# Kernel tuning notes

Measured on AMD Instinct MI355X. Metric: run time of the kernel, lower is better.

The kernel has to match this reference:

```python
import jax, jax.numpy as jnp
import numpy as np

B, N, IN_DIM, OUT_DIM = 8, 2048, 256, 256
EDGE_P = 0.02   # adjacency density
MASK_P = 0.9    # fraction of valid nodes


def setup_inputs() -> dict:
    key = jax.random.key(0)
    ks = jax.random.split(key, 8)
    x = jax.random.normal(ks[0], (B, N, IN_DIM), dtype=jnp.float32)
    adj = (jax.random.uniform(ks[1], (B, N, N)) < EDGE_P).astype(jnp.float32)
    mask = (jax.random.uniform(ks[2], (B, N)) < MASK_P).astype(jnp.float32)
    # nn.Linear(in_dim, out_dim): W [out, in], b [out]
    lim1 = 1.0 / np.sqrt(IN_DIM)
    W = jax.random.uniform(ks[3], (OUT_DIM, IN_DIM), minval=-lim1, maxval=lim1, dtype=jnp.float32)
    b = jax.random.uniform(ks[4], (OUT_DIM,), minval=-lim1, maxval=lim1, dtype=jnp.float32)
    # nn.Linear(2*out_dim, 1): weight [1, 2D] split into a1 (acts on h_i), a2 (acts on h_j)
    lim2 = 1.0 / np.sqrt(2 * OUT_DIM)
    a1 = jax.random.uniform(ks[5], (OUT_DIM,), minval=-lim2, maxval=lim2, dtype=jnp.float32)
    a2 = jax.random.uniform(ks[6], (OUT_DIM,), minval=-lim2, maxval=lim2, dtype=jnp.float32)
    att_b = jax.random.uniform(ks[7], (), minval=-lim2, maxval=lim2, dtype=jnp.float32)
    return {"x": x, "adj": adj, "mask": mask, "W": W, "b": b, "a1": a1, "a2": a2, "att_b": att_b}


def reference(x, adj, mask, W, b, a1, a2, att_b):
    # h = Linear(x): [B, N, D]
    h = jnp.einsum('bni,di->bnd', x, W) + b
    # attention(cat([h_i, h_j])) == h_i @ a1 + h_j @ a2 + att_b (linear in each half)
    s1 = h @ a1  # [B, N] -> contributes along i
    s2 = h @ a2  # [B, N] -> contributes along j
    logits = s1[:, :, None] + s2[:, None, :] + att_b  # [B, N, N]
    att = jax.nn.sigmoid(logits) * adj
    att = att * mask[:, :, None] * mask[:, None, :]
    att = att / (jnp.sum(att, axis=-1, keepdims=True) + 1e-8)
    h_new = jnp.einsum('bij,bjd->bid', att, h)
    return h_new * mask[:, :, None]
```

## Files before the change

### kernel.cpp

```cpp
#include <hip/hip_runtime.h>
#include <hip/hip_bf16.h>

#define BB 8
#define NN 2048
#define DD 256
#define MM (BB * NN)

typedef __attribute__((ext_vector_type(8))) short bf16x8_t;
typedef __attribute__((ext_vector_type(4))) float f32x4_t;

__global__ __launch_bounds__(256) void gemm_h(
    const float* __restrict__ x,
    const float* __restrict__ Wt,
    const float* __restrict__ bias,
    __hip_bfloat16* __restrict__ h)
{
    __shared__ __hip_bfloat16 As[64][72];
    __shared__ __hip_bfloat16 Bs[64][72];

    const int tid  = threadIdx.x;
    const int r    = tid >> 2;
    const int cs   = (tid & 3) * 16;
    const int w    = tid >> 6;
    const int lane = tid & 63;
    const int m16  = lane & 15;
    const int quad = lane >> 4;
    const long rowBase = (long)blockIdx.x * 64;
    const int  colBase = blockIdx.y * 64;

    f32x4_t acc[4];
#pragma unroll
    for (int c = 0; c < 4; c++) acc[c] = (f32x4_t){0.f, 0.f, 0.f, 0.f};

    for (int k0 = 0; k0 < 256; k0 += 64) {
        const float4* ag = (const float4*)(x  + (rowBase + r) * 256 + k0 + cs);
        const float4* bg = (const float4*)(Wt + (long)(colBase + r) * 256 + k0 + cs);
        float4 av[4], bv[4];
#pragma unroll
        for (int q = 0; q < 4; q++) { av[q] = ag[q]; bv[q] = bg[q]; }

        __align__(16) __hip_bfloat16 ta[16], tb[16];
#pragma unroll
        for (int q = 0; q < 4; q++) {
            ta[q * 4 + 0] = __float2bfloat16(av[q].x);
            ta[q * 4 + 1] = __float2bfloat16(av[q].y);
            ta[q * 4 + 2] = __float2bfloat16(av[q].z);
            ta[q * 4 + 3] = __float2bfloat16(av[q].w);
            tb[q * 4 + 0] = __float2bfloat16(bv[q].x);
            tb[q * 4 + 1] = __float2bfloat16(bv[q].y);
            tb[q * 4 + 2] = __float2bfloat16(bv[q].z);
            tb[q * 4 + 3] = __float2bfloat16(bv[q].w);
        }

        __syncthreads();
        *(uint4*)&As[r][cs]     = *(uint4*)&ta[0];
        *(uint4*)&As[r][cs + 8] = *(uint4*)&ta[8];
        *(uint4*)&Bs[r][cs]     = *(uint4*)&tb[0];
        *(uint4*)&Bs[r][cs + 8] = *(uint4*)&tb[8];
        __syncthreads();

#pragma unroll
        for (int kk = 0; kk < 64; kk += 32) {
            bf16x8_t af = *(const bf16x8_t*)&As[w * 16 + m16][kk + quad * 8];
#pragma unroll
            for (int c = 0; c < 4; c++) {
                bf16x8_t bf = *(const bf16x8_t*)&Bs[c * 16 + m16][kk + quad * 8];
                acc[c] = __builtin_amdgcn_mfma_f32_16x16x32_bf16(af, bf, acc[c], 0, 0, 0);
            }
        }
    }

#pragma unroll
    for (int c = 0; c < 4; c++) {
        const int col = colBase + c * 16 + m16;
        const float bv = bias[col];
#pragma unroll
        for (int reg = 0; reg < 4; reg++) {
            const long row = rowBase + w * 16 + quad * 4 + reg;
            h[row * 256 + col] = __float2bfloat16(acc[c][reg] + bv);
        }
    }
}

struct __attribute__((aligned(8))) bf4 { __hip_bfloat16 v[4]; };

__global__ __launch_bounds__(256) void s_kernel(
    const __hip_bfloat16* __restrict__ h,
    const float* __restrict__ a1,
    const float* __restrict__ a2,
    const float* __restrict__ mask,
    const float* __restrict__ attb_p,
    float* __restrict__ s1b, float* __restrict__ t2)
{
    const int w = threadIdx.x >> 6;
    const int lane = threadIdx.x & 63;
    const long row = (long)blockIdx.x * 4 + w;

    bf4 hv = *(const bf4*)(h + row * 256 + lane * 4);
    float4 A1 = *(const float4*)(a1 + lane * 4);
    float4 A2 = *(const float4*)(a2 + lane * 4);
    const float h0 = __bfloat162float(hv.v[0]), h1 = __bfloat162float(hv.v[1]);
    const float h2 = __bfloat162float(hv.v[2]), h3 = __bfloat162float(hv.v[3]);
    float p1 = h0 * A1.x + h1 * A1.y + h2 * A1.z + h3 * A1.w;
    float p2 = h0 * A2.x + h1 * A2.y + h2 * A2.z + h3 * A2.w;
#pragma unroll
    for (int off = 32; off; off >>= 1) {
        p1 += __shfl_down(p1, off);
        p2 += __shfl_down(p2, off);
    }
    if (lane == 0) {
        s1b[row] = p1 + attb_p[0];
        t2[row]  = (mask[row] != 0.f) ? p2 : -1e30f;
    }
}

__global__ __launch_bounds__(256, 8) void attn_agg(
    const float* __restrict__ adj,
    const float* __restrict__ mask,
    const __hip_bfloat16* __restrict__ h,
    const float* __restrict__ s1b,
    const float* __restrict__ t2,
    float* __restrict__ out)
{
    __shared__ float2 s_list[2048];
    __shared__ int    s_cnt;
    __shared__ float  s_sum[4];

    const int tid  = threadIdx.x;
    const int wv   = tid >> 6;
    const int lane = tid & 63;
    const int b    = blockIdx.x & 7;
    const int i    = blockIdx.x >> 3;
    const long row   = (long)b * NN + i;
    const long mbase = (long)b * NN;

    const float mask_i = mask[row];
    if (mask_i == 0.f) {
        out[row * 256 + tid] = 0.f;
        return;
    }
    if (tid == 0) s_cnt = 0;
    __syncthreads();

    const float si = s1b[row];
    const float4* arow = (const float4*)(adj + row * NN);
    const float4* trow = (const float4*)(t2 + mbase);

    float4 A0 = arow[tid], A1 = arow[256 + tid];
    float4 T0 = trow[tid], T1 = trow[256 + tid];

    float lsum = 0.f;
#pragma unroll
    for (int g = 0; g < 2; g++) {
        const int jb = (g * 1024 + tid * 4) << 9;
        const float av[4] = {g ? A1.x : A0.x, g ? A1.y : A0.y, g ? A1.z : A0.z, g ? A1.w : A0.w};
        const float tv[4] = {g ? T1.x : T0.x, g ? T1.y : T0.y, g ? T1.z : T0.z, g ? T1.w : T0.w};
#pragma unroll
        for (int e = 0; e < 4; e++) {
            const float z   = si + tv[e];
            const float sig = __builtin_amdgcn_rcpf(1.f + __expf(-z));
            const float wgt = av[e] * sig;
            lsum += wgt;
            if (wgt != 0.f) {
                const int pos = atomicAdd(&s_cnt, 1);
                s_list[pos] = make_float2(__int_as_float(jb + (e << 9)), wgt);
            }
        }
    }

#pragma unroll
    for (int off = 32; off; off >>= 1) lsum += __shfl_down(lsum, off);
    if (lane == 0) s_sum[wv] = lsum;
    __syncthreads();

    const float inv = 1.f / (s_sum[0] + s_sum[1] + s_sum[2] + s_sum[3] + 1e-8f);
    const int   cnt = s_cnt;

    const char* hb   = (const char*)(h + mbase * 256);
    const int   coff = tid * 2;
    float acc = 0.f;
    int k = 0;
    for (; k + 8 <= cnt; k += 8) {
        float4 e[4];
#pragma unroll
        for (int q = 0; q < 4; q++) e[q] = *(const float4*)&s_list[k + q * 2];
        unsigned short u[8];
#pragma unroll
        for (int q = 0; q < 4; q++) {
            u[q * 2]     = *(const unsigned short*)(hb + __float_as_int(e[q].x) + coff);
            u[q * 2 + 1] = *(const unsigned short*)(hb + __float_as_int(e[q].z) + coff);
        }
#pragma unroll
        for (int q = 0; q < 4; q++) {
            acc += e[q].y * __uint_as_float(((unsigned)u[q * 2]) << 16);
            acc += e[q].w * __uint_as_float(((unsigned)u[q * 2 + 1]) << 16);
        }
    }
    for (; k + 2 <= cnt; k += 2) {
        float4 e = *(const float4*)&s_list[k];
        unsigned short u0 = *(const unsigned short*)(hb + __float_as_int(e.x) + coff);
        unsigned short u1 = *(const unsigned short*)(hb + __float_as_int(e.z) + coff);
        acc += e.y * __uint_as_float(((unsigned)u0) << 16);
        acc += e.w * __uint_as_float(((unsigned)u1) << 16);
    }
    if (k < cnt) {
        float2 e = s_list[k];
        unsigned short u = *(const unsigned short*)(hb + __float_as_int(e.x) + coff);
        acc += e.y * __uint_as_float(((unsigned)u) << 16);
    }

    out[row * 256 + tid] = acc * inv;
}

extern "C" void kernel_launch(void* const* d_in, const int* in_sizes, int n_in,
                              void* d_out, int out_size, void* d_ws, size_t ws_size,
                              hipStream_t stream) {
    const float* x    = (const float*)d_in[0];
    const float* adj  = (const float*)d_in[1];
    const float* mask = (const float*)d_in[2];
    const float* W    = (const float*)d_in[3];
    const float* bias = (const float*)d_in[4];
    const float* a1   = (const float*)d_in[5];
    const float* a2   = (const float*)d_in[6];
    const float* attb = (const float*)d_in[7];
    float* out = (float*)d_out;

    __hip_bfloat16* h = (__hip_bfloat16*)d_ws;
    float* s1b = (float*)((char*)d_ws + (size_t)MM * DD * 2);
    float* t2  = s1b + MM;

    gemm_h<<<dim3(MM / 64, DD / 64), 256, 0, stream>>>(x, W, bias, h);
    s_kernel<<<MM / 4, 256, 0, stream>>>(h, a1, a2, mask, attb, s1b, t2);
    attn_agg<<<MM, 256, 0, stream>>>(adj, mask, h, s1b, t2, out);
}
```

Before: 256.9 us.

## Split neighbor gather across wavefronts with 4-wide bf16 loads and LDS reduction

The aggregation loop now divides the neighbor list among the four wavefronts. Each lane loads 8 bytes (4 bf16 columns) per neighbor row instead of one 2-byte value, and the per-wave partial sums are combined through shared memory. The neighbor list is stored as separate ushort index and float weight arrays. This cuts the number of tiny global loads and the per-thread loop length, at the cost of an extra barrier, a 4 KB LDS partial buffer and higher LDS use that may lower occupancy.

After: 239.8 us. -6.6%, faster.

```diff
diff --git a/kernel.cpp b/kernel.cpp
--- a/kernel.cpp
+++ b/kernel.cpp
@@ -122,9 +122,11 @@
     const float* __restrict__ t2,
     float* __restrict__ out)
 {
-    __shared__ float2 s_list[2048];
-    __shared__ int    s_cnt;
-    __shared__ float  s_sum[4];
+    __shared__ unsigned short s_j[2048];
+    __shared__ float          s_w[2048];
+    __shared__ float          s_part[4][DD];
+    __shared__ int            s_cnt;
+    __shared__ float          s_sum[4];
 
     const int tid  = threadIdx.x;
     const int wv   = tid >> 6;
@@ -152,7 +154,7 @@
     float lsum = 0.f;
 #pragma unroll
     for (int g = 0; g < 2; g++) {
-        const int jb = (g * 1024 + tid * 4) << 9;
+        const int jb = g * 1024 + tid * 4;
         const float av[4] = {g ? A1.x : A0.x, g ? A1.y : A0.y, g ? A1.z : A0.z, g ? A1.w : A0.w};
         const float tv[4] = {g ? T1.x : T0.x, g ? T1.y : T0.y, g ? T1.z : T0.z, g ? T1.w : T0.w};
 #pragma unroll
@@ -163,7 +165,8 @@
             lsum += wgt;
             if (wgt != 0.f) {
                 const int pos = atomicAdd(&s_cnt, 1);
-                s_list[pos] = make_float2(__int_as_float(jb + (e << 9)), wgt);
+                s_j[pos] = (unsigned short)(jb + e);
+                s_w[pos] = wgt;
             }
         }
     }
@@ -176,40 +179,69 @@
     const float inv = 1.f / (s_sum[0] + s_sum[1] + s_sum[2] + s_sum[3] + 1e-8f);
     const int   cnt = s_cnt;
 
+    const int qs = ((cnt + 15) >> 4) << 2;
+    const int ks = min(wv * qs, cnt);
+    const int ke = min(ks + qs, cnt);
     const char* hb   = (const char*)(h + mbase * 256);
-    const int   coff = tid * 2;
-    float acc = 0.f;
-    int k = 0;
-    for (; k + 8 <= cnt; k += 8) {
-        float4 e[4];
-#pragma unroll
-        for (int q = 0; q < 4; q++) e[q] = *(const float4*)&s_list[k + q * 2];
-        unsigned short u[8];
+    const int   loff = lane * 8;
+
+    float c0 = 0.f, c1 = 0.f, c2 = 0.f, c3 = 0.f;
+    int k = ks;
+    for (; k + 8 <= ke; k += 8) {
+        ushort4 ja = *(const ushort4*)&s_j[k];
+        ushort4 jb2 = *(const ushort4*)&s_j[k + 4];
+        float4  wa = *(const float4*)&s_w[k];
+        float4  wb = *(const float4*)&s_w[k + 4];
+        uint2 u[8];
+        u[0] = *(const uint2*)(hb + ((int)ja.x  << 9) + loff);
+        u[1] = *(const uint2*)(hb + ((int)ja.y  << 9) + loff);
+        u[2] = *(const uint2*)(hb + ((int)ja.z  << 9) + loff);
+        u[3] = *(const uint2*)(hb + ((int)ja.w  << 9) + loff);
+        u[4] = *(const uint2*)(hb + ((int)jb2.x << 9) + loff);
+        u[5] = *(const uint2*)(hb + ((int)jb2.y << 9) + loff);
+        u[6] = *(const uint2*)(hb + ((int)jb2.z << 9) + loff);
+        u[7] = *(const uint2*)(hb + ((int)jb2.w << 9) + loff);
+        const float ww[8] = {wa.x, wa.y, wa.z, wa.w, wb.x, wb.y, wb.z, wb.w};
+#pragma unroll
+        for (int q = 0; q < 8; q++) {
+            c0 += ww[q] * __uint_as_float(u[q].x << 16);
+            c1 += ww[q] * __uint_as_float(u[q].x & 0xffff0000u);
+            c2 += ww[q] * __uint_as_float(u[q].y << 16);
+            c3 += ww[q] * __uint_as_float(u[q].y & 0xffff0000u);
+        }
+    }
+    for (; k + 4 <= ke; k += 4) {
+        ushort4 ja = *(const ushort4*)&s_j[k];
+        float4  wa = *(const float4*)&s_w[k];
+        uint2 u[4];
+        u[0] = *(const uint2*)(hb + ((int)ja.x << 9) + loff);
+        u[1] = *(const uint2*)(hb + ((int)ja.y << 9) + loff);
+        u[2] = *(const uint2*)(hb + ((int)ja.z << 9) + loff);
+        u[3] = *(const uint2*)(hb + ((int)ja.w << 9) + loff);
+        const float ww[4] = {wa.x, wa.y, wa.z, wa.w};
 #pragma unroll
         for (int q = 0; q < 4; q++) {
-            u[q * 2]     = *(const unsigned short*)(hb + __float_as_int(e[q].x) + coff);
-            u[q * 2 + 1] = *(const unsigned short*)(hb + __float_as_int(e[q].z) + coff);
-        }
-#pragma unroll
-        for (int q = 0; q < 4; q++) {
-            acc += e[q].y * __uint_as_float(((unsigned)u[q * 2]) << 16);
-            acc += e[q].w * __uint_as_float(((unsigned)u[q * 2 + 1]) << 16);
-        }
-    }
-    for (; k + 2 <= cnt; k += 2) {
-        float4 e = *(const float4*)&s_list[k];
-        unsigned short u0 = *(const unsigned short*)(hb + __float_as_int(e.x) + coff);
-        unsigned short u1 = *(const unsigned short*)(hb + __float_as_int(e.z) + coff);
-        acc += e.y * __uint_as_float(((unsigned)u0) << 16);
-        acc += e.w * __uint_as_float(((unsigned)u1) << 16);
-    }
-    if (k < cnt) {
-        float2 e = s_list[k];
-        unsigned short u = *(const unsigned short*)(hb + __float_as_int(e.x) + coff);
-        acc += e.y * __uint_as_float(((unsigned)u) << 16);
-    }
-
-    out[row * 256 + tid] = acc * inv;
+            c0 += ww[q] * __uint_as_float(u[q].x << 16);
+            c1 += ww[q] * __uint_as_float(u[q].x & 0xffff0000u);
+            c2 += ww[q] * __uint_as_float(u[q].y << 16);
+            c3 += ww[q] * __uint_as_float(u[q].y & 0xffff0000u);
+        }
+    }
+    for (; k < ke; k++) {
+        const int jj = s_j[k];
+        const float wk = s_w[k];
+        uint2 u = *(const uint2*)(hb + (jj << 9) + loff);
+        c0 += wk * __uint_as_float(u.x << 16);
+        c1 += wk * __uint_as_float(u.x & 0xffff0000u);
+        c2 += wk * __uint_as_float(u.y << 16);
+        c3 += wk * __uint_as_float(u.y & 0xffff0000u);
+    }
+
+    *(float4*)&s_part[wv][lane * 4] = make_float4(c0, c1, c2, c3);
+    __syncthreads();
+
+    const float total = s_part[0][tid] + s_part[1][tid] + s_part[2][tid] + s_part[3][tid];
+    out[row * 256 + tid] = total * inv;
 }
 
 extern "C" void kernel_launch(void* const* d_in, const int* in_sizes, int n_in,
```

## Replace sparse gather aggregation with dense MFMA attention matmul over transposed h

Applied to the files above, without the earlier changes.

The per-row sparse gather kernel, which compacted nonzero attention weights into shared memory and gathered h rows, is replaced by a dense tiled matmul. Each block builds a 32x64 bf16 tile of attention weights from adj and the sigmoid logits, then multiplies it with a transposed copy of h using MFMA. The GEMM now also writes that transposed copy. This removes the LDS atomics, the irregular scattered 2-byte loads and the one-block-per-row launch. In exchange it does about 50x more FLOPs, since the adjacency is only ~2% dense, rounds the attention weights to bf16, and computes masked rows instead of skipping them.

Measured after the change: 286.8 us. 11.7% more time.

```diff
diff --git a/kernel.cpp b/kernel.cpp
--- a/kernel.cpp
+++ b/kernel.cpp
@@ -13,7 +13,8 @@
     const float* __restrict__ x,
     const float* __restrict__ Wt,
     const float* __restrict__ bias,
-    __hip_bfloat16* __restrict__ h)
+    __hip_bfloat16* __restrict__ h,
+    __hip_bfloat16* __restrict__ hT)
 {
     __shared__ __hip_bfloat16 As[64][72];
     __shared__ __hip_bfloat16 Bs[64][72];
@@ -70,15 +71,21 @@
         }
     }
 
+    const long r0 = rowBase + w * 16 + quad * 4;
+    const int  bb = (int)(r0 >> 11);
+    const int  ib = (int)(r0 & 2047);
 #pragma unroll
     for (int c = 0; c < 4; c++) {
         const int col = colBase + c * 16 + m16;
         const float bv = bias[col];
-#pragma unroll
-        for (int reg = 0; reg < 4; reg++) {
-            const long row = rowBase + w * 16 + quad * 4 + reg;
-            h[row * 256 + col] = __float2bfloat16(acc[c][reg] + bv);
-        }
+        union { ushort4 u; __hip_bfloat16 b[4]; } pk;
+#pragma unroll
+        for (int reg = 0; reg < 4; reg++)
+            pk.b[reg] = __float2bfloat16(acc[c][reg] + bv);
+#pragma unroll
+        for (int reg = 0; reg < 4; reg++)
+            h[(r0 + reg) * 256 + col] = pk.b[reg];
+        *(ushort4*)((unsigned short*)hT + ((long)bb * 256 + col) * 2048 + ib) = pk.u;
     }
 }
 
@@ -114,102 +121,95 @@
     }
 }
 
-__global__ __launch_bounds__(256, 8) void attn_agg(
+__global__ __launch_bounds__(256, 2) void attn_mm(
     const float* __restrict__ adj,
     const float* __restrict__ mask,
-    const __hip_bfloat16* __restrict__ h,
+    const __hip_bfloat16* __restrict__ hT,
     const float* __restrict__ s1b,
     const float* __restrict__ t2,
     float* __restrict__ out)
 {
-    __shared__ float2 s_list[2048];
-    __shared__ int    s_cnt;
-    __shared__ float  s_sum[4];
+    __shared__ __hip_bfloat16 Ps[32][72];
+    __shared__ float s_dinv[32];
 
     const int tid  = threadIdx.x;
     const int wv   = tid >> 6;
     const int lane = tid & 63;
+    const int m16  = lane & 15;
+    const int quad = lane >> 4;
     const int b    = blockIdx.x & 7;
-    const int i    = blockIdx.x >> 3;
-    const long row   = (long)b * NN + i;
+    const int i0   = (blockIdx.x >> 3) * 32;
     const long mbase = (long)b * NN;
 
-    const float mask_i = mask[row];
-    if (mask_i == 0.f) {
-        out[row * 256 + tid] = 0.f;
-        return;
-    }
-    if (tid == 0) s_cnt = 0;
-    __syncthreads();
-
-    const float si = s1b[row];
-    const float4* arow = (const float4*)(adj + row * NN);
-    const float4* trow = (const float4*)(t2 + mbase);
-
-    float4 A0 = arow[tid], A1 = arow[256 + tid];
-    float4 T0 = trow[tid], T1 = trow[256 + tid];
-
-    float lsum = 0.f;
-#pragma unroll
-    for (int g = 0; g < 2; g++) {
-        const int jb = (g * 1024 + tid * 4) << 9;
-        const float av[4] = {g ? A1.x : A0.x, g ? A1.y : A0.y, g ? A1.z : A0.z, g ? A1.w : A0.w};
-        const float tv[4] = {g ? T1.x : T0.x, g ? T1.y : T0.y, g ? T1.z : T0.z, g ? T1.w : T0.w};
-#pragma unroll
-        for (int e = 0; e < 4; e++) {
+    const int sr = tid >> 3;
+    const int sc = (tid & 7) * 8;
+    const float si = s1b[mbase + i0 + sr];
+    const float* adjrow = adj + (mbase + i0 + sr) * (long)NN;
+    const float* t2p    = t2 + mbase;
+    const __hip_bfloat16* hTb = hT + (long)b * 256 * NN;
+
+    f32x4_t acc[2][4];
+#pragma unroll
+    for (int hh = 0; hh < 2; hh++)
+#pragma unroll
+        for (int c = 0; c < 4; c++) acc[hh][c] = (f32x4_t){0.f, 0.f, 0.f, 0.f};
+    float dsum = 0.f;
+
+    for (int k0 = 0; k0 < NN; k0 += 64) {
+        float4 a0 = *(const float4*)(adjrow + k0 + sc);
+        float4 a1 = *(const float4*)(adjrow + k0 + sc + 4);
+        float4 t0 = *(const float4*)(t2p + k0 + sc);
+        float4 t1 = *(const float4*)(t2p + k0 + sc + 4);
+        const float av[8] = {a0.x, a0.y, a0.z, a0.w, a1.x, a1.y, a1.z, a1.w};
+        const float tv[8] = {t0.x, t0.y, t0.z, t0.w, t1.x, t1.y, t1.z, t1.w};
+        union { uint4 v; __hip_bfloat16 bf[8]; } pk;
+#pragma unroll
+        for (int e = 0; e < 8; e++) {
             const float z   = si + tv[e];
             const float sig = __builtin_amdgcn_rcpf(1.f + __expf(-z));
-            const float wgt = av[e] * sig;
-            lsum += wgt;
-            if (wgt != 0.f) {
-                const int pos = atomicAdd(&s_cnt, 1);
-                s_list[pos] = make_float2(__int_as_float(jb + (e << 9)), wgt);
+            pk.bf[e] = __float2bfloat16(av[e] * sig);
+            dsum += __bfloat162float(pk.bf[e]);
+        }
+        __syncthreads();
+        *(uint4*)&Ps[sr][sc] = pk.v;
+        __syncthreads();
+
+#pragma unroll
+        for (int kh = 0; kh < 2; kh++) {
+            bf16x8_t bf0 = *(const bf16x8_t*)&Ps[m16][kh * 32 + quad * 8];
+            bf16x8_t bf1 = *(const bf16x8_t*)&Ps[16 + m16][kh * 32 + quad * 8];
+#pragma unroll
+            for (int c = 0; c < 4; c++) {
+                const int d = wv * 64 + c * 16 + m16;
+                bf16x8_t af = *(const bf16x8_t*)(hTb + (long)d * NN + k0 + kh * 32 + quad * 8);
+                acc[0][c] = __builtin_amdgcn_mfma_f32_16x16x32_bf16(af, bf0, acc[0][c], 0, 0, 0);
+                acc[1][c] = __builtin_amdgcn_mfma_f32_16x16x32_bf16(af, bf1, acc[1][c], 0, 0, 0);
             }
         }
     }
 
-#pragma unroll
-    for (int off = 32; off; off >>= 1) lsum += __shfl_down(lsum, off);
-    if (lane == 0) s_sum[wv] = lsum;
+    dsum += __shfl_down(dsum, 4);
+    dsum += __shfl_down(dsum, 2);
+    dsum += __shfl_down(dsum, 1);
+    if ((lane & 7) == 0) {
+        const int rr = wv * 8 + (lane >> 3);
+        const float mk = mask[mbase + i0 + rr];
+        s_dinv[rr] = (mk != 0.f) ? 1.f / (dsum + 1e-8f) : 0.f;
+    }
     __syncthreads();
 
-    const float inv = 1.f / (s_sum[0] + s_sum[1] + s_sum[2] + s_sum[3] + 1e-8f);
-    const int   cnt = s_cnt;
-
-    const char* hb   = (const char*)(h + mbase * 256);
-    const int   coff = tid * 2;
-    float acc = 0.f;
-    int k = 0;
-    for (; k + 8 <= cnt; k += 8) {
-        float4 e[4];
-#pragma unroll
-        for (int q = 0; q < 4; q++) e[q] = *(const float4*)&s_list[k + q * 2];
-        unsigned short u[8];
-#pragma unroll
-        for (int q = 0; q < 4; q++) {
-            u[q * 2]     = *(const unsigned short*)(hb + __float_as_int(e[q].x) + coff);
-            u[q * 2 + 1] = *(const unsigned short*)(hb + __float_as_int(e[q].z) + coff);
-        }
-#pragma unroll
-        for (int q = 0; q < 4; q++) {
-            acc += e[q].y * __uint_as_float(((unsigned)u[q * 2]) << 16);
-            acc += e[q].w * __uint_as_float(((unsigned)u[q * 2 + 1]) << 16);
-        }
-    }
-    for (; k + 2 <= cnt; k += 2) {
-        float4 e = *(const float4*)&s_list[k];
-        unsigned short u0 = *(const unsigned short*)(hb + __float_as_int(e.x) + coff);
-        unsigned short u1 = *(const unsigned short*)(hb + __float_as_int(e.z) + coff);
-        acc += e.y * __uint_as_float(((unsigned)u0) << 16);
-        acc += e.w * __uint_as_float(((unsigned)u1) << 16);
-    }
-    if (k < cnt) {
-        float2 e = s_list[k];
-        unsigned short u = *(const unsigned short*)(hb + __float_as_int(e.x) + coff);
-        acc += e.y * __uint_as_float(((unsigned)u) << 16);
-    }
-
-    out[row * 256 + tid] = acc * inv;
+#pragma unroll
+    for (int hh = 0; hh < 2; hh++) {
+        const float dinv = s_dinv[hh * 16 + m16];
+        float* orow = out + (mbase + i0 + hh * 16 + m16) * 256;
+#pragma unroll
+        for (int c = 0; c < 4; c++) {
+            const int d = wv * 64 + c * 16 + quad * 4;
+            float4 v = make_float4(acc[hh][c][0] * dinv, acc[hh][c][1] * dinv,
+                                   acc[hh][c][2] * dinv, acc[hh][c][3] * dinv);
+            *(float4*)(orow + d) = v;
+        }
+    }
 }
 
 extern "C" void kernel_launch(void* const* d_in, const int* in_sizes, int n_in,
@@ -225,11 +225,12 @@
     const float* attb = (const float*)d_in[7];
     float* out = (float*)d_out;
 
-    __hip_bfloat16* h = (__hip_bfloat16*)d_ws;
-    float* s1b = (float*)((char*)d_ws + (size_t)MM * DD * 2);
+    __hip_bfloat16* h  = (__hip_bfloat16*)d_ws;
+    __hip_bfloat16* hT = h + (size_t)MM * DD;
+    float* s1b = (float*)((char*)d_ws + 2 * (size_t)MM * DD * 2);
     float* t2  = s1b + MM;
 
-    gemm_h<<<dim3(MM / 64, DD / 64), 256, 0, stream>>>(x, W, bias, h);
+    gemm_h<<<dim3(MM / 64, DD / 64), 256, 0, stream>>>(x, W, bias, h, hT);
     s_kernel<<<MM / 4, 256, 0, stream>>>(h, a1, a2, mask, attb, s1b, t2);
-    attn_agg<<<MM, 256, 0, stream>>>(adj, mask, h, s1b, t2, out);
-}
+    attn_mm<<<MM / 32, 256, 0, stream>>>(adj, mask, hT, s1b, t2, out);
+}
```
